# Kernel tuning notes

Measured on AMD Instinct MI355X. Metric: run time of the kernel, lower is better.

The kernel has to match this reference:

```python
import jax, jax.numpy as jnp
import numpy as np

VOCAB, X_SIZE, H_SIZE, N_CLASSES = 50000, 300, 150, 5
DEPTH = 18                      # complete binary tree, N = 2^(DEPTH+1)-1 nodes
N_NODES = 2 ** (DEPTH + 1) - 1  # 524287
SCALE = 0.05                    # param init scale for numerical sanity


def setup_inputs() -> dict:
    key = jax.random.key(0)
    ks = jax.random.split(key, 8)
    return {
        "x_id": jax.random.randint(ks[0], (N_NODES,), 0, VOCAB, dtype=jnp.int32),
        "emb": jax.random.normal(ks[1], (VOCAB, X_SIZE), jnp.float32) * SCALE,
        "W_iou": jax.random.normal(ks[2], (X_SIZE, 3 * H_SIZE), jnp.float32) * SCALE,
        "U_iou": jax.random.normal(ks[3], (H_SIZE, 3 * H_SIZE), jnp.float32) * SCALE,
        "b_iou": jnp.zeros((3 * H_SIZE,), jnp.float32),
        "W_f": jax.random.normal(ks[4], (X_SIZE, H_SIZE), jnp.float32) * SCALE,
        "U_f": jax.random.normal(ks[5], (H_SIZE, H_SIZE), jnp.float32) * SCALE,
        "b_f": jnp.zeros((H_SIZE,), jnp.float32),
        "W_out": jax.random.normal(ks[6], (H_SIZE, N_CLASSES), jnp.float32) * SCALE,
        "b_out": jnp.zeros((N_CLASSES,), jnp.float32),
    }


def reference(x_id, emb, W_iou, U_iou, b_iou, W_f, U_f, b_f, W_out, b_out):
    # Child-Sum TreeLSTM propagated leaves->root over a complete binary tree
    # stored in heap layout: children of node i are 2i+1, 2i+2.
    N = x_id.shape[0]
    H = U_iou.shape[0]
    depth = int(np.log2(N + 1)) - 1

    x = emb[x_id]  # input_module: embedding lookup  [N, X]
    h = jnp.zeros((N, H), x.dtype)
    c = jnp.zeros((N, H), x.dtype)

    # level-batched topological propagation (19 static levels)
    for lvl in range(depth, -1, -1):
        s, e = 2 ** lvl - 1, 2 ** (lvl + 1) - 1  # node range of this level
        xl = x[s:e]                              # [n_l, X]
        if lvl == depth:  # leaves: zero child state
            h_sum = jnp.zeros((e - s, H), x.dtype)
            fc_sum = jnp.zeros((e - s, H), x.dtype)
        else:
            # children of consecutive nodes are contiguous: [2s+1, 2e+1)
            hc = h[2 * s + 1:2 * e + 1].reshape(e - s, 2, H)
            cc = c[2 * s + 1:2 * e + 1].reshape(e - s, 2, H)
            h_sum = hc.sum(axis=1)               # reduce: sum child h
            # per-child forget gate
            f = jax.nn.sigmoid((xl @ W_f)[:, None, :] + hc @ U_f + b_f)
            fc_sum = (f * cc).sum(axis=1)
        iou = xl @ W_iou + h_sum @ U_iou + b_iou  # [n_l, 3H]
        i, o, u = jnp.split(iou, 3, axis=-1)
        c_new = jax.nn.sigmoid(i) * jnp.tanh(u) + fc_sum
        h_new = jax.nn.sigmoid(o) * jnp.tanh(c_new)
        h = h.at[s:e].set(h_new)
        c = c.at[s:e].set(c_new)

    return h @ W_out + b_out  # output_module: Linear(H, C)  [N, C]
```

## Files before the change

### kernel.cpp

```cpp
#include <hip/hip_runtime.h>
#include <cstdint>

typedef _Float16 f16_t;
typedef __attribute__((ext_vector_type(8))) _Float16 f16x8;
typedef __attribute__((ext_vector_type(4))) _Float16 f16x4;
typedef __attribute__((ext_vector_type(4))) float f32x4;

#define HP      160
#define NCOL    640
#define KXP     320
#define NNODES  524287
#define LEAF_S  262143
#define LEAF_M  262144
#define NVOCAB  50000
#define AST     168

__device__ __forceinline__ float frcp(float x) { return __builtin_amdgcn_rcpf(x); }
__device__ __forceinline__ float sigf(float x) { return frcp(1.0f + __expf(-x)); }
__device__ __forceinline__ float tanhf_(float x) {
  return 1.0f - 2.0f * frcp(1.0f + __expf(2.0f * x));
}
__device__ __forceinline__ f16x8 zero8() {
  f16x8 z;
#pragma unroll
  for (int i = 0; i < 8; ++i) z[i] = (_Float16)0.0f;
  return z;
}
__device__ __forceinline__ f32x4 zero4() {
  f32x4 z;
#pragma unroll
  for (int i = 0; i < 4; ++i) z[i] = 0.0f;
  return z;
}

__global__ void prep_params(const float* __restrict__ W_iou, const float* __restrict__ U_iou,
                            const float* __restrict__ b_iou, const float* __restrict__ W_f,
                            const float* __restrict__ U_f, const float* __restrict__ b_f,
                            f16_t* __restrict__ WreT, f16_t* __restrict__ UreT,
                            float* __restrict__ bre) {
  int idx = blockIdx.x * 256 + threadIdx.x;
  if (idx < NCOL * KXP) {
    int col = idx / KXP, k = idx % KXP;
    int j = col >> 2, g = col & 3;
    float v = 0.0f;
    if (k < 300 && j < 150) v = (g < 3) ? W_iou[k * 450 + g * 150 + j] : W_f[k * 150 + j];
    WreT[idx] = (f16_t)v;
  } else if (idx < NCOL * KXP + NCOL * HP) {
    int i2 = idx - NCOL * KXP;
    int col = i2 / HP, k = i2 % HP;
    int g = col / 160, j = col % 160;
    float v = 0.0f;
    if (k < 150 && j < 150) v = (g < 3) ? U_iou[k * 450 + g * 150 + j] : U_f[k * 150 + j];
    UreT[i2] = (f16_t)v;
  } else if (idx < NCOL * KXP + NCOL * HP + NCOL) {
    int col = idx - (NCOL * KXP + NCOL * HP);
    int j = col >> 2, g = col & 3;
    bre[col] = (j < 150) ? ((g < 3) ? b_iou[g * 150 + j] : b_f[j]) : 0.0f;
  }
}

__global__ __launch_bounds__(256) void gemm_p(const float* __restrict__ emb,
                                              const f16_t* __restrict__ WreT,
                                              const float* __restrict__ bre,
                                              f16_t* __restrict__ P) {
  __shared__ __align__(16) f16_t A_sh[64 * 328];
  __shared__ __align__(16) f16_t B_sh[128 * 40];
  const int tid = threadIdx.x;
  const int wid = tid >> 6, lane = tid & 63, l15 = lane & 15, q = lane >> 4;
  const int row0 = blockIdx.x * 64;

#pragma unroll
  for (int i = 0; i < 10; ++i) {
    int ch = tid + 256 * i;
    int r = ch / 40, kc = (ch % 40) * 8;
    int grow = row0 + r;
    f16x8 hv;
    if (grow < NVOCAB && kc + 8 <= 300) {
      float4 a = *(const float4*)&emb[grow * 300 + kc];
      float4 b = *(const float4*)&emb[grow * 300 + kc + 4];
      hv[0] = (_Float16)a.x; hv[1] = (_Float16)a.y; hv[2] = (_Float16)a.z; hv[3] = (_Float16)a.w;
      hv[4] = (_Float16)b.x; hv[5] = (_Float16)b.y; hv[6] = (_Float16)b.z; hv[7] = (_Float16)b.w;
    } else {
#pragma unroll
      for (int e = 0; e < 8; ++e) {
        int k = kc + e;
        float v = (grow < NVOCAB && k < 300) ? emb[grow * 300 + k] : 0.0f;
        hv[e] = (_Float16)v;
      }
    }
    *(f16x8*)&A_sh[r * 328 + kc] = hv;
  }
  __syncthreads();

  for (int bn = 0; bn < 5; ++bn) {
    const int col0 = bn * 128;
    f32x4 acc[8];
#pragma unroll
    for (int t = 0; t < 8; ++t) acc[t] = zero4();
    for (int kk = 0; kk < KXP; kk += 32) {
#pragma unroll
      for (int i = 0; i < 2; ++i) {
        int ch = tid + 256 * i;
        int cidx = ch >> 2, kc = (ch & 3) * 8;
        *(f16x8*)&B_sh[cidx * 40 + kc] =
            *(const f16x8*)&WreT[(col0 + cidx) * KXP + kk + kc];
      }
      __syncthreads();
      f16x8 af = *(const f16x8*)&A_sh[(16 * wid + l15) * 328 + kk + q * 8];
#pragma unroll
      for (int t = 0; t < 8; ++t) {
        f16x8 bfr = *(const f16x8*)&B_sh[(t * 16 + l15) * 40 + q * 8];
        acc[t] = __builtin_amdgcn_mfma_f32_16x16x32_f16(af, bfr, acc[t], 0, 0, 0);
      }
      __syncthreads();
    }
#pragma unroll
    for (int t = 0; t < 8; ++t) {
      int col = col0 + t * 16 + l15;
      float bias = bre[col];
#pragma unroll
      for (int r2 = 0; r2 < 4; ++r2) {
        int row = row0 + 16 * wid + q * 4 + r2;
        if (row < NVOCAB) P[(long)row * NCOL + col] = (f16_t)(acc[t][r2] + bias);
      }
    }
  }
}

__global__ void leafhc_kernel(const f16_t* __restrict__ P, f16_t* __restrict__ Hleaf,
                              f16_t* __restrict__ Cleaf) {
  int idx = blockIdx.x * 256 + threadIdx.x;
  if (idx >= NVOCAB * 80) return;
  int v = idx / 80, t = idx % 80;
  f16x8 pk = *(const f16x8*)&P[(long)v * NCOL + t * 8];
#pragma unroll
  for (int e = 0; e < 2; ++e) {
    float iv = (float)pk[e * 4 + 0], ov = (float)pk[e * 4 + 1], uv = (float)pk[e * 4 + 2];
    float cl = sigf(iv) * tanhf_(uv);
    float hl = sigf(ov) * tanhf_(cl);
    Hleaf[(long)v * HP + t * 2 + e] = (f16_t)hl;
    Cleaf[(long)v * HP + t * 2 + e] = (f16_t)cl;
  }
}

__global__ void oleaf_kernel(const f16_t* __restrict__ Hleaf, const float* __restrict__ W_out,
                             const float* __restrict__ b_out, float* __restrict__ Oleaf) {
  const int tid = threadIdx.x;
  const int row = blockIdx.x * 16 + (tid >> 4), l = tid & 15;
  if (row >= NVOCAB) return;
  float acc[5] = {0, 0, 0, 0, 0};
  for (int j = l; j < 150; j += 16) {
    float hv = (float)Hleaf[(long)row * HP + j];
#pragma unroll
    for (int m = 0; m < 5; ++m) acc[m] += hv * W_out[j * 5 + m];
  }
#pragma unroll
  for (int m = 0; m < 5; ++m) {
    float vv = acc[m];
    vv += __shfl_xor(vv, 1);
    vv += __shfl_xor(vv, 2);
    vv += __shfl_xor(vv, 4);
    vv += __shfl_xor(vv, 8);
    if (l == 0) Oleaf[(long)row * 8 + m] = vv + b_out[m];
  }
}

__global__ void leafout_kernel(const int* __restrict__ x_id, const float* __restrict__ Oleaf,
                               float* __restrict__ out) {
  int leaf = blockIdx.x * 256 + threadIdx.x;
  int xv = x_id[LEAF_S + leaf];
  const float* O = Oleaf + (long)xv * 8;
  float4 o4 = *(const float4*)O;
  float o5 = O[4];
  long base = ((long)LEAF_S + leaf) * 5;
  out[base + 0] = o4.x; out[base + 1] = o4.y; out[base + 2] = o4.z;
  out[base + 3] = o4.w; out[base + 4] = o5;
}

__global__ __launch_bounds__(256, 3) void level17b_kernel(
    const int* __restrict__ x_id, const f16_t* __restrict__ P,
    const f16_t* __restrict__ UreT, const f16_t* __restrict__ Hleaf,
    const f16_t* __restrict__ Cleaf, f16_t* __restrict__ Hout,
    f16_t* __restrict__ Cout, const float* __restrict__ W_out,
    const float* __restrict__ b_out, float* __restrict__ out) {
  __shared__ __align__(16) f16_t A_sh[128 * AST];
  __shared__ __align__(16) f16_t B_sh[128 * 40];
  const int tid = threadIdx.x;
  const int wid = tid >> 6, lane = tid & 63, l15 = lane & 15, q = lane >> 4;
  const int p0 = blockIdx.x * 64;
  const int s1 = (1 << 17) - 1;
  const long childbase = 2L * s1 + 1 + 2 * p0;

#pragma unroll
  for (int i = 0; i < 10; ++i) {
    int ch = tid + 256 * i;
    int r = ch / 20, kc = (ch % 20) * 8;
    int xv = x_id[childbase + r];
    *(f16x8*)&A_sh[r * AST + kc] = *(const f16x8*)&Hleaf[(long)xv * HP + kc];
  }
  __syncthreads();

  int xvp[2][2], xvl[2][2], xvr[2][2];
#pragma unroll
  for (int mt = 0; mt < 2; ++mt)
#pragma unroll
    for (int rr = 0; rr < 2; ++rr) {
      int pl = 16 * wid + 8 * mt + 2 * q + rr;
      xvp[mt][rr] = x_id[(long)s1 + p0 + pl];
      xvl[mt][rr] = x_id[childbase + 2 * pl];
      xvr[mt][rr] = x_id[childbase + 2 * pl + 1];
    }
  float oacc[2][2][5] = {};

  for (int jt = 0; jt < 5; ++jt) {
    const int j0 = jt * 32;
    f32x4 acc[2][4][2];
#pragma unroll
    for (int mt = 0; mt < 2; ++mt)
#pragma unroll
      for (int g = 0; g < 4; ++g)
#pragma unroll
        for (int jh = 0; jh < 2; ++jh) acc[mt][g][jh] = zero4();

    for (int kk = 0; kk < HP; kk += 32) {
#pragma unroll
      for (int i = 0; i < 2; ++i) {
        int ch = tid + 256 * i;
        int cidx = ch >> 2, kc = (ch & 3) * 8;
        int g = cidx >> 5, jj = cidx & 31;
        int col = g * HP + j0 + jj;
        *(f16x8*)&B_sh[cidx * 40 + kc] = *(const f16x8*)&UreT[col * HP + kk + kc];
      }
      __syncthreads();
      f16x8 af0 = *(const f16x8*)&A_sh[(32 * wid + l15) * AST + kk + q * 8];
      f16x8 af1 = *(const f16x8*)&A_sh[(32 * wid + 16 + l15) * AST + kk + q * 8];
#pragma unroll
      for (int g = 0; g < 4; ++g)
#pragma unroll
        for (int jh = 0; jh < 2; ++jh) {
          f16x8 bfr = *(const f16x8*)&B_sh[(g * 32 + jh * 16 + l15) * 40 + q * 8];
          acc[0][g][jh] = __builtin_amdgcn_mfma_f32_16x16x32_f16(af0, bfr, acc[0][g][jh], 0, 0, 0);
          acc[1][g][jh] = __builtin_amdgcn_mfma_f32_16x16x32_f16(af1, bfr, acc[1][g][jh], 0, 0, 0);
        }
      __syncthreads();
    }

#pragma unroll
    for (int mt = 0; mt < 2; ++mt)
#pragma unroll
      for (int rr = 0; rr < 2; ++rr) {
        const int r = rr * 2;
        const int pl = 16 * wid + 8 * mt + 2 * q + rr;
        const f16_t* Prp = P + (long)xvp[mt][rr] * NCOL;
#pragma unroll
        for (int jh = 0; jh < 2; ++jh) {
          const int j = j0 + jh * 16 + l15;
          f16x4 pp = *(const f16x4*)&Prp[j * 4];
          float ipre = (float)pp[0] + acc[mt][0][jh][r] + acc[mt][0][jh][r + 1];
          float opre = (float)pp[1] + acc[mt][1][jh][r] + acc[mt][1][jh][r + 1];
          float upre = (float)pp[2] + acc[mt][2][jh][r] + acc[mt][2][jh][r + 1];
          float pf   = (float)pp[3];
          float fl = sigf(pf + acc[mt][3][jh][r]);
          float fr = sigf(pf + acc[mt][3][jh][r + 1]);
          float clv = (float)Cleaf[(long)xvl[mt][rr] * HP + j];
          float crv = (float)Cleaf[(long)xvr[mt][rr] * HP + j];
          float cn = sigf(ipre) * tanhf_(upre) + fl * clv + fr * crv;
          float hn = sigf(opre) * tanhf_(cn);
          Hout[(long)(p0 + pl) * HP + j] = (f16_t)hn;
          Cout[(long)(p0 + pl) * HP + j] = (f16_t)cn;
          int wbase = (j < 150) ? j * 5 : 0;
#pragma unroll
          for (int m = 0; m < 5; ++m) oacc[mt][rr][m] += hn * W_out[wbase + m];
        }
      }
  }

#pragma unroll
  for (int mt = 0; mt < 2; ++mt)
#pragma unroll
    for (int rr = 0; rr < 2; ++rr) {
      int pl = 16 * wid + 8 * mt + 2 * q + rr;
#pragma unroll
      for (int m = 0; m < 5; ++m) {
        float v = oacc[mt][rr][m];
        v += __shfl_xor(v, 1);
        v += __shfl_xor(v, 2);
        v += __shfl_xor(v, 4);
        v += __shfl_xor(v, 8);
        if (l15 == 0) out[((long)s1 + p0 + pl) * 5 + m] = v + b_out[m];
      }
    }
}

template <bool LEAF>
__global__ __launch_bounds__(256, 3) void fused_kernel(
    const int* __restrict__ x_id, const f16_t* __restrict__ P,
    const f16_t* __restrict__ UreT, const f16_t* __restrict__ Hc,
    const f16_t* __restrict__ Cc, f16_t* __restrict__ Hout,
    f16_t* __restrict__ Cout, const float* __restrict__ W_out,
    const float* __restrict__ b_out, float* __restrict__ out, int s1, int M1) {
  __shared__ __align__(16) f16_t A_sh[64 * AST];
  __shared__ __align__(16) f16_t A2_sh[32 * AST];
  __shared__ __align__(16) f16_t B_sh[128 * 40];
  __shared__ f16_t C_sh[32 * 160];
  const int tid = threadIdx.x;
  const int wid = tid >> 6, lane = tid & 63, l15 = lane & 15, q = lane >> 4;
  const int p0 = blockIdx.x * 32;
  const long childbase = 2L * s1 + 1 + 2 * p0;

#pragma unroll
  for (int i = 0; i < 5; ++i) {
    int ch = tid + 256 * i;
    int r = ch / 20, kc = (ch % 20) * 8;
    f16x8 v;
    if (LEAF) {
      int xv = x_id[childbase + r];
      v = *(const f16x8*)&Hc[(long)xv * HP + kc];
    } else {
      v = *(const f16x8*)&Hc[(long)(2 * p0 + r) * HP + kc];
    }
    *(f16x8*)&A_sh[r * AST + kc] = v;
  }
  __syncthreads();

  int xvp[2], xvl[2], xvr[2];
#pragma unroll
  for (int rr = 0; rr < 2; ++rr) {
    int pl = 8 * wid + 2 * q + rr;
    long pn = (long)s1 + p0 + pl;
    xvp[rr] = x_id[pn];
    if (LEAF) {
      xvl[rr] = x_id[childbase + 2 * pl];
      xvr[rr] = x_id[childbase + 2 * pl + 1];
    }
  }
  float oacc1[2][5] = {};

  for (int jt = 0; jt < 5; ++jt) {
    const int j0 = jt * 32;
    f32x4 acc[4][2];
#pragma unroll
    for (int g = 0; g < 4; ++g)
#pragma unroll
      for (int jh = 0; jh < 2; ++jh) acc[g][jh] = zero4();

    for (int kk = 0; kk < HP; kk += 32) {
#pragma unroll
      for (int i = 0; i < 2; ++i) {
        int ch = tid + 256 * i;
        int cidx = ch >> 2, kc = (ch & 3) * 8;
        int g = cidx >> 5, jj = cidx & 31;
        int col = g * HP + j0 + jj;
        *(f16x8*)&B_sh[cidx * 40 + kc] = *(const f16x8*)&UreT[col * HP + kk + kc];
      }
      __syncthreads();
      f16x8 af = *(const f16x8*)&A_sh[(16 * wid + l15) * AST + kk + q * 8];
#pragma unroll
      for (int g = 0; g < 4; ++g)
#pragma unroll
        for (int jh = 0; jh < 2; ++jh) {
          f16x8 bfr = *(const f16x8*)&B_sh[(g * 32 + jh * 16 + l15) * 40 + q * 8];
          acc[g][jh] = __builtin_amdgcn_mfma_f32_16x16x32_f16(af, bfr, acc[g][jh], 0, 0, 0);
        }
      __syncthreads();
    }

#pragma unroll
    for (int rr = 0; rr < 2; ++rr) {
      const int r = rr * 2;
      const int lr0 = 16 * wid + q * 4 + r;
      const int pl = lr0 >> 1;
      const f16_t* Prp = P + (long)xvp[rr] * NCOL;
#pragma unroll
      for (int jh = 0; jh < 2; ++jh) {
        const int j = j0 + jh * 16 + l15;
        f16x4 pp = *(const f16x4*)&Prp[j * 4];
        float ipre = (float)pp[0] + acc[0][jh][r] + acc[0][jh][r + 1];
        float opre = (float)pp[1] + acc[1][jh][r] + acc[1][jh][r + 1];
        float upre = (float)pp[2] + acc[2][jh][r] + acc[2][jh][r + 1];
        float pf   = (float)pp[3];
        float fl = sigf(pf + acc[3][jh][r]);
        float fr = sigf(pf + acc[3][jh][r + 1]);
        float clv, crv;
        if (LEAF) {
          clv = (float)Cc[(long)xvl[rr] * HP + j];
          crv = (float)Cc[(long)xvr[rr] * HP + j];
        } else {
          clv = (float)Cc[(long)(2 * p0 + lr0) * HP + j];
          crv = (float)Cc[(long)(2 * p0 + lr0 + 1) * HP + j];
        }
        float cn = sigf(ipre) * tanhf_(upre) + fl * clv + fr * crv;
        float hn = sigf(opre) * tanhf_(cn);
        A2_sh[pl * AST + j] = (f16_t)hn;
        C_sh[pl * 160 + j] = (f16_t)cn;
        int wbase = (j < 150) ? j * 5 : 0;
#pragma unroll
        for (int m = 0; m < 5; ++m) oacc1[rr][m] += hn * W_out[wbase + m];
      }
    }
  }

#pragma unroll
  for (int rr = 0; rr < 2; ++rr) {
    int pl = 8 * wid + 2 * q + rr;
#pragma unroll
    for (int m = 0; m < 5; ++m) {
      float v = oacc1[rr][m];
      v += __shfl_xor(v, 1);
      v += __shfl_xor(v, 2);
      v += __shfl_xor(v, 4);
      v += __shfl_xor(v, 8);
      if (l15 == 0) out[((long)s1 + p0 + pl) * 5 + m] = v + b_out[m];
    }
  }

  const int s2 = (s1 - 1) >> 1;
  const int p02 = p0 >> 1;
  const bool act2 = (wid < 2);
  int xvp2[2];
#pragma unroll
  for (int rr = 0; rr < 2; ++rr) {
    int pl = 8 * wid + 2 * q + rr;
    long pn = (long)s2 + p02 + (act2 ? pl : 0);
    xvp2[rr] = x_id[pn];
  }
  float oacc2[2][5] = {};

  for (int jt = 0; jt < 5; ++jt) {
    const int j0 = jt * 32;
    f32x4 acc[4][2];
#pragma unroll
    for (int g = 0; g < 4; ++g)
#pragma unroll
      for (int jh = 0; jh < 2; ++jh) acc[g][jh] = zero4();

    for (int kk = 0; kk < HP; kk += 32) {
#pragma unroll
      for (int i = 0; i < 2; ++i) {
        int ch = tid + 256 * i;
        int cidx = ch >> 2, kc = (ch & 3) * 8;
        int g = cidx >> 5, jj = cidx & 31;
        int col = g * HP + j0 + jj;
        *(f16x8*)&B_sh[cidx * 40 + kc] = *(const f16x8*)&UreT[col * HP + kk + kc];
      }
      __syncthreads();
      if (act2) {
        f16x8 af = *(const f16x8*)&A2_sh[(16 * wid + l15) * AST + kk + q * 8];
#pragma unroll
        for (int g = 0; g < 4; ++g)
#pragma unroll
          for (int jh = 0; jh < 2; ++jh) {
            f16x8 bfr = *(const f16x8*)&B_sh[(g * 32 + jh * 16 + l15) * 40 + q * 8];
            acc[g][jh] = __builtin_amdgcn_mfma_f32_16x16x32_f16(af, bfr, acc[g][jh], 0, 0, 0);
          }
      }
      __syncthreads();
    }

    if (act2) {
#pragma unroll
      for (int rr = 0; rr < 2; ++rr) {
        const int r = rr * 2;
        const int lr0 = 16 * wid + q * 4 + r;
        const int pl = lr0 >> 1;
        const f16_t* Prp = P + (long)xvp2[rr] * NCOL;
#pragma unroll
        for (int jh = 0; jh < 2; ++jh) {
          const int j = j0 + jh * 16 + l15;
          f16x4 pp = *(const f16x4*)&Prp[j * 4];
          float ipre = (float)pp[0] + acc[0][jh][r] + acc[0][jh][r + 1];
          float opre = (float)pp[1] + acc[1][jh][r] + acc[1][jh][r + 1];
          float upre = (float)pp[2] + acc[2][jh][r] + acc[2][jh][r + 1];
          float pf   = (float)pp[3];
          float fl = sigf(pf + acc[3][jh][r]);
          float fr = sigf(pf + acc[3][jh][r + 1]);
          float clv = (float)C_sh[lr0 * 160 + j];
          float crv = (float)C_sh[(lr0 + 1) * 160 + j];
          float cn = sigf(ipre) * tanhf_(upre) + fl * clv + fr * crv;
          float hn = sigf(opre) * tanhf_(cn);
          Hout[(long)(p02 + pl) * HP + j] = (f16_t)hn;
          Cout[(long)(p02 + pl) * HP + j] = (f16_t)cn;
          int wbase = (j < 150) ? j * 5 : 0;
#pragma unroll
          for (int m = 0; m < 5; ++m) oacc2[rr][m] += hn * W_out[wbase + m];
        }
      }
    }
  }

  if (act2) {
#pragma unroll
    for (int rr = 0; rr < 2; ++rr) {
      int pl = 8 * wid + 2 * q + rr;
#pragma unroll
      for (int m = 0; m < 5; ++m) {
        float v = oacc2[rr][m];
        v += __shfl_xor(v, 1);
        v += __shfl_xor(v, 2);
        v += __shfl_xor(v, 4);
        v += __shfl_xor(v, 8);
        if (l15 == 0) out[((long)s2 + p02 + pl) * 5 + m] = v + b_out[m];
      }
    }
  }
}

__device__ __forceinline__ void level_tile(
    const int* __restrict__ x_id, const f16_t* __restrict__ P,
    const f16_t* __restrict__ UreT, const f16_t* __restrict__ h_child,
    const f16_t* __restrict__ c_child, f16_t* __restrict__ h_par,
    f16_t* __restrict__ c_par, const float* Wo, const float* __restrict__ b_out,
    float* __restrict__ out, int s, int M, int p0, f16_t* A_sh, f16_t* B_sh) {
  const int tid = threadIdx.x;
  const int wid = tid >> 6, lane = tid & 63, l15 = lane & 15, q = lane >> 4;
  int rowsValid = 2 * M - 2 * p0;
  if (rowsValid > 64) rowsValid = 64;

#pragma unroll
  for (int i = 0; i < 5; ++i) {
    int ch = tid + 256 * i;
    int r = ch / 20, kc = (ch % 20) * 8;
    f16x8 v;
    if (r < rowsValid) v = *(const f16x8*)&h_child[(long)(2 * p0 + r) * HP + kc];
    else v = zero8();
    *(f16x8*)&A_sh[r * 184 + kc] = v;
  }
  __syncthreads();

  int xvp[2]; long pnode[2]; int plg[2]; bool valid[2]; int lr0v[2];
#pragma unroll
  for (int rr = 0; rr < 2; ++rr) {
    int lr0 = 16 * wid + q * 4 + rr * 2;
    int pl = lr0 >> 1;
    valid[rr] = (p0 + pl) < M;
    long pn = (long)s + p0 + (valid[rr] ? pl : 0);
    pnode[rr] = pn; plg[rr] = p0 + pl; lr0v[rr] = lr0;
    xvp[rr] = x_id[pn];
  }

  float oacc[2][5];
#pragma unroll
  for (int rr = 0; rr < 2; ++rr)
#pragma unroll
    for (int m = 0; m < 5; ++m) oacc[rr][m] = 0.0f;

  for (int jt = 0; jt < 5; ++jt) {
    const int j0 = jt * 32;
    f32x4 acc[4][2];
#pragma unroll
    for (int g = 0; g < 4; ++g)
#pragma unroll
      for (int jh = 0; jh < 2; ++jh) acc[g][jh] = zero4();

    for (int kk = 0; kk < HP; kk += 32) {
#pragma unroll
      for (int i = 0; i < 2; ++i) {
        int ch = tid + 256 * i;
        int cidx = ch >> 2, kc = (ch & 3) * 8;
        int g = cidx >> 5, jj = cidx & 31;
        int col = g * HP + j0 + jj;
        *(f16x8*)&B_sh[cidx * 40 + kc] = *(const f16x8*)&UreT[col * HP + kk + kc];
      }
      __syncthreads();
      f16x8 af = *(const f16x8*)&A_sh[(16 * wid + l15) * 184 + kk + q * 8];
#pragma unroll
      for (int g = 0; g < 4; ++g)
#pragma unroll
        for (int jh = 0; jh < 2; ++jh) {
          f16x8 bfr = *(const f16x8*)&B_sh[(g * 32 + jh * 16 + l15) * 40 + q * 8];
          acc[g][jh] = __builtin_amdgcn_mfma_f32_16x16x32_f16(af, bfr, acc[g][jh], 0, 0, 0);
        }
      __syncthreads();
    }

#pragma unroll
    for (int rr = 0; rr < 2; ++rr) {
      const int r = rr * 2;
      const f16_t* Prp = P + (long)xvp[rr] * NCOL;
#pragma unroll
      for (int jh = 0; jh < 2; ++jh) {
        const int j = j0 + jh * 16 + l15;
        f16x4 pp = *(const f16x4*)&Prp[j * 4];
        float ipre = (float)pp[0] + acc[0][jh][r] + acc[0][jh][r + 1];
        float opre = (float)pp[1] + acc[1][jh][r] + acc[1][jh][r + 1];
        float upre = (float)pp[2] + acc[2][jh][r] + acc[2][jh][r + 1];
        float pf   = (float)pp[3];
        float fl = sigf(pf + acc[3][jh][r]);
        float fr = sigf(pf + acc[3][jh][r + 1]);
        float clv = valid[rr] ? (float)c_child[(long)(2 * p0 + lr0v[rr]) * HP + j] : 0.0f;
        float crv = valid[rr] ? (float)c_child[(long)(2 * p0 + lr0v[rr] + 1) * HP + j] : 0.0f;
        float cn = sigf(ipre) * tanhf_(upre) + fl * clv + fr * crv;
        float hn = sigf(opre) * tanhf_(cn);
        if (valid[rr]) {
          h_par[(long)plg[rr] * HP + j] = (f16_t)hn;
          c_par[(long)plg[rr] * HP + j] = (f16_t)cn;
        }
#pragma unroll
        for (int m = 0; m < 5; ++m) oacc[rr][m] += hn * Wo[j * 5 + m];
      }
    }
  }

#pragma unroll
  for (int rr = 0; rr < 2; ++rr) {
#pragma unroll
    for (int m = 0; m < 5; ++m) {
      float v = oacc[rr][m];
      v += __shfl_xor(v, 1);
      v += __shfl_xor(v, 2);
      v += __shfl_xor(v, 4);
      v += __shfl_xor(v, 8);
      if (l15 == 0 && valid[rr]) out[pnode[rr] * 5 + m] = v + b_out[m];
    }
  }
}

__global__ __launch_bounds__(256, 4) void tail_kernel(
    const int* __restrict__ x_id, const f16_t* __restrict__ P,
    const f16_t* __restrict__ UreT, f16_t* __restrict__ HA, f16_t* __restrict__ HB,
    f16_t* __restrict__ CA, f16_t* __restrict__ CB, const float* __restrict__ W_out,
    const float* __restrict__ b_out, float* __restrict__ out) {
  __shared__ __align__(16) f16_t A_sh[64 * 184];
  __shared__ __align__(16) f16_t B_sh[128 * 40];
  __shared__ float Wo[800];
  for (int i = threadIdx.x; i < 800; i += 256) Wo[i] = (i < 750) ? W_out[i] : 0.0f;
  for (int lvl = 4; lvl >= 0; --lvl) {
    int s = (1 << lvl) - 1, M = 1 << lvl;
    const f16_t* hc = ((lvl + 1) & 1) ? HA : HB;
    const f16_t* cc = ((lvl + 1) & 1) ? CA : CB;
    f16_t* hp = (lvl & 1) ? HA : HB;
    f16_t* cp = (lvl & 1) ? CA : CB;
    level_tile(x_id, P, UreT, hc, cc, hp, cp, Wo, b_out, out, s, M, 0, A_sh, B_sh);
    __syncthreads();
  }
}

extern "C" void kernel_launch(void* const* d_in, const int* in_sizes, int n_in,
                              void* d_out, int out_size, void* d_ws, size_t ws_size,
                              hipStream_t stream) {
  const int* x_id   = (const int*)d_in[0];
  const float* emb  = (const float*)d_in[1];
  const float* W_iou = (const float*)d_in[2];
  const float* U_iou = (const float*)d_in[3];
  const float* b_iou = (const float*)d_in[4];
  const float* W_f   = (const float*)d_in[5];
  const float* U_f   = (const float*)d_in[6];
  const float* b_f   = (const float*)d_in[7];
  const float* W_out = (const float*)d_in[8];
  const float* b_out = (const float*)d_in[9];
  float* out = (float*)d_out;
  char* ws = (char*)d_ws;

  f16_t* WreT  = (f16_t*)(ws + 0);
  f16_t* UreT  = (f16_t*)(ws + 409600);
  float* bre   = (float*)(ws + 614400);
  f16_t* P     = (f16_t*)(ws + 616960);
  f16_t* Hleaf = (f16_t*)(ws + 64616960);
  f16_t* Cleaf = (f16_t*)(ws + 80616960);
  float* Oleaf = (float*)(ws + 96616960);
  f16_t* H17   = (f16_t*)(ws + 96616960);
  f16_t* C17   = (f16_t*)(ws + 138560000);
  f16_t* H15 = (f16_t*)(ws + 64616960);
  f16_t* C15 = (f16_t*)(ws + 75102720);
  f16_t* H13 = (f16_t*)(ws + 96616960);
  f16_t* C13 = (f16_t*)(ws + 99238400);
  f16_t* H11 = (f16_t*)(ws + 64616960);
  f16_t* C11 = (f16_t*)(ws + 65272320);
  f16_t* H9  = (f16_t*)(ws + 96616960);
  f16_t* C9  = (f16_t*)(ws + 96780800);
  f16_t* H7  = (f16_t*)(ws + 64616960);
  f16_t* C7  = (f16_t*)(ws + 64657920);
  f16_t* H5  = (f16_t*)(ws + 96616960);
  f16_t* C5  = (f16_t*)(ws + 96627200);
  f16_t* HSc = (f16_t*)(ws + 64616960);
  f16_t* CSc = (f16_t*)(ws + 64627200);

  prep_params<<<1203, 256, 0, stream>>>(W_iou, U_iou, b_iou, W_f, U_f, b_f, WreT, UreT, bre);
  gemm_p<<<782, 256, 0, stream>>>(emb, WreT, bre, P);
  leafhc_kernel<<<15625, 256, 0, stream>>>(P, Hleaf, Cleaf);
  oleaf_kernel<<<3125, 256, 0, stream>>>(Hleaf, W_out, b_out, Oleaf);
  leafout_kernel<<<1024, 256, 0, stream>>>(x_id, Oleaf, out);

  level17b_kernel<<<2048, 256, 0, stream>>>(x_id, P, UreT, Hleaf, Cleaf, H17, C17,
                                            W_out, b_out, out);
  fused_kernel<false><<<2048, 256, 0, stream>>>(x_id, P, UreT, H17, C17, H15, C15,
                                                W_out, b_out, out, (1 << 16) - 1, 1 << 16);
  fused_kernel<false><<<512, 256, 0, stream>>>(x_id, P, UreT, H15, C15, H13, C13,
                                               W_out, b_out, out, (1 << 14) - 1, 1 << 14);
  fused_kernel<false><<<128, 256, 0, stream>>>(x_id, P, UreT, H13, C13, H11, C11,
                                               W_out, b_out, out, (1 << 12) - 1, 1 << 12);
  fused_kernel<false><<<32, 256, 0, stream>>>(x_id, P, UreT, H11, C11, H9, C9,
                                              W_out, b_out, out, (1 << 10) - 1, 1 << 10);
  fused_kernel<false><<<8, 256, 0, stream>>>(x_id, P, UreT, H9, C9, H7, C7,
                                             W_out, b_out, out, (1 << 8) - 1, 1 << 8);
  fused_kernel<false><<<2, 256, 0, stream>>>(x_id, P, UreT, H7, C7, H5, C5,
                                             W_out, b_out, out, (1 << 6) - 1, 1 << 6);
  tail_kernel<<<1, 256, 0, stream>>>(x_id, P, UreT, H5, HSc, C5, CSc, W_out, b_out, out);

  (void)in_sizes; (void)n_in; (void)out_size; (void)ws_size;
}
```

Before: 814.5 us.

## Fuse leaf h/c/output kernels and widen two-level fused kernel tiles

Merges the leaf h/c kernel and leaf output-projection kernel into one pass over P. The leaf output scatter now runs at the end of the level-17 kernel, and Oleaf moves to its own workspace region. The two-level fused kernel now handles 64 parents per block, so the second level uses all four waves instead of two, with level-one h/c staged in shared memory. This removes two launches and an Hleaf reread and improves wave utilisation, at the cost of more registers (hreg/creg arrays) and half as many blocks per level.

```diff
diff --git a/kernel.cpp b/kernel.cpp
--- a/kernel.cpp
+++ b/kernel.cpp
@@ -4,6 +4,7 @@
 typedef _Float16 f16_t;
 typedef __attribute__((ext_vector_type(8))) _Float16 f16x8;
 typedef __attribute__((ext_vector_type(4))) _Float16 f16x4;
+typedef __attribute__((ext_vector_type(2))) _Float16 f16x2;
 typedef __attribute__((ext_vector_type(4))) float f32x4;
 
 #define HP      160
@@ -127,36 +128,29 @@
   }
 }
 
-__global__ void leafhc_kernel(const f16_t* __restrict__ P, f16_t* __restrict__ Hleaf,
-                              f16_t* __restrict__ Cleaf) {
-  int idx = blockIdx.x * 256 + threadIdx.x;
-  if (idx >= NVOCAB * 80) return;
-  int v = idx / 80, t = idx % 80;
-  f16x8 pk = *(const f16x8*)&P[(long)v * NCOL + t * 8];
-#pragma unroll
-  for (int e = 0; e < 2; ++e) {
-    float iv = (float)pk[e * 4 + 0], ov = (float)pk[e * 4 + 1], uv = (float)pk[e * 4 + 2];
+__global__ void leafhco_kernel(const f16_t* __restrict__ P, const float* __restrict__ W_out,
+                               const float* __restrict__ b_out, f16_t* __restrict__ Hleaf,
+                               f16_t* __restrict__ Cleaf, float* __restrict__ Oleaf) {
+  const int tid = threadIdx.x;
+  const int row = blockIdx.x * 16 + (tid >> 4), l = tid & 15;
+  const f16_t* Pr = P + (long)row * NCOL;
+  float oacc[5] = {0, 0, 0, 0, 0};
+#pragma unroll
+  for (int jj = 0; jj < 10; ++jj) {
+    int j = jj * 16 + l;
+    f16x4 pp = *(const f16x4*)&Pr[j * 4];
+    float iv = (float)pp[0], ov = (float)pp[1], uv = (float)pp[2];
     float cl = sigf(iv) * tanhf_(uv);
     float hl = sigf(ov) * tanhf_(cl);
-    Hleaf[(long)v * HP + t * 2 + e] = (f16_t)hl;
-    Cleaf[(long)v * HP + t * 2 + e] = (f16_t)cl;
-  }
-}
-
-__global__ void oleaf_kernel(const f16_t* __restrict__ Hleaf, const float* __restrict__ W_out,
-                             const float* __restrict__ b_out, float* __restrict__ Oleaf) {
-  const int tid = threadIdx.x;
-  const int row = blockIdx.x * 16 + (tid >> 4), l = tid & 15;
-  if (row >= NVOCAB) return;
-  float acc[5] = {0, 0, 0, 0, 0};
-  for (int j = l; j < 150; j += 16) {
-    float hv = (float)Hleaf[(long)row * HP + j];
-#pragma unroll
-    for (int m = 0; m < 5; ++m) acc[m] += hv * W_out[j * 5 + m];
+    Hleaf[(long)row * HP + j] = (f16_t)hl;
+    Cleaf[(long)row * HP + j] = (f16_t)cl;
+    int wbase = (j < 150) ? j * 5 : 0;
+#pragma unroll
+    for (int m = 0; m < 5; ++m) oacc[m] += hl * W_out[wbase + m];
   }
 #pragma unroll
   for (int m = 0; m < 5; ++m) {
-    float vv = acc[m];
+    float vv = oacc[m];
     vv += __shfl_xor(vv, 1);
     vv += __shfl_xor(vv, 2);
     vv += __shfl_xor(vv, 4);
@@ -165,24 +159,13 @@
   }
 }
 
-__global__ void leafout_kernel(const int* __restrict__ x_id, const float* __restrict__ Oleaf,
-                               float* __restrict__ out) {
-  int leaf = blockIdx.x * 256 + threadIdx.x;
-  int xv = x_id[LEAF_S + leaf];
-  const float* O = Oleaf + (long)xv * 8;
-  float4 o4 = *(const float4*)O;
-  float o5 = O[4];
-  long base = ((long)LEAF_S + leaf) * 5;
-  out[base + 0] = o4.x; out[base + 1] = o4.y; out[base + 2] = o4.z;
-  out[base + 3] = o4.w; out[base + 4] = o5;
-}
-
 __global__ __launch_bounds__(256, 3) void level17b_kernel(
     const int* __restrict__ x_id, const f16_t* __restrict__ P,
     const f16_t* __restrict__ UreT, const f16_t* __restrict__ Hleaf,
-    const f16_t* __restrict__ Cleaf, f16_t* __restrict__ Hout,
-    f16_t* __restrict__ Cout, const float* __restrict__ W_out,
-    const float* __restrict__ b_out, float* __restrict__ out) {
+    const f16_t* __restrict__ Cleaf, const float* __restrict__ Oleaf,
+    f16_t* __restrict__ Hout, f16_t* __restrict__ Cout,
+    const float* __restrict__ W_out, const float* __restrict__ b_out,
+    float* __restrict__ out) {
   __shared__ __align__(16) f16_t A_sh[128 * AST];
   __shared__ __align__(16) f16_t B_sh[128 * 40];
   const int tid = threadIdx.x;
@@ -290,59 +273,60 @@
         if (l15 == 0) out[((long)s1 + p0 + pl) * 5 + m] = v + b_out[m];
       }
     }
-}
-
-template <bool LEAF>
-__global__ __launch_bounds__(256, 3) void fused_kernel(
+
+  if (tid < 128) {
+    long leaf = childbase + tid;
+    int xv = x_id[leaf];
+    const float* O = Oleaf + (long)xv * 8;
+    float4 o4 = *(const float4*)O;
+    float o5 = O[4];
+    long base = leaf * 5;
+    out[base + 0] = o4.x; out[base + 1] = o4.y; out[base + 2] = o4.z;
+    out[base + 3] = o4.w; out[base + 4] = o5;
+  }
+}
+
+__global__ __launch_bounds__(256, 3) void fusedb_kernel(
     const int* __restrict__ x_id, const f16_t* __restrict__ P,
     const f16_t* __restrict__ UreT, const f16_t* __restrict__ Hc,
     const f16_t* __restrict__ Cc, f16_t* __restrict__ Hout,
     f16_t* __restrict__ Cout, const float* __restrict__ W_out,
-    const float* __restrict__ b_out, float* __restrict__ out, int s1, int M1) {
-  __shared__ __align__(16) f16_t A_sh[64 * AST];
-  __shared__ __align__(16) f16_t A2_sh[32 * AST];
+    const float* __restrict__ b_out, float* __restrict__ out, int s1) {
+  __shared__ __align__(16) f16_t A_sh[128 * AST];
   __shared__ __align__(16) f16_t B_sh[128 * 40];
-  __shared__ f16_t C_sh[32 * 160];
   const int tid = threadIdx.x;
   const int wid = tid >> 6, lane = tid & 63, l15 = lane & 15, q = lane >> 4;
-  const int p0 = blockIdx.x * 32;
-  const long childbase = 2L * s1 + 1 + 2 * p0;
-
-#pragma unroll
-  for (int i = 0; i < 5; ++i) {
+  const int p0 = blockIdx.x * 64;
+
+#pragma unroll
+  for (int i = 0; i < 10; ++i) {
     int ch = tid + 256 * i;
     int r = ch / 20, kc = (ch % 20) * 8;
-    f16x8 v;
-    if (LEAF) {
-      int xv = x_id[childbase + r];
-      v = *(const f16x8*)&Hc[(long)xv * HP + kc];
-    } else {
-      v = *(const f16x8*)&Hc[(long)(2 * p0 + r) * HP + kc];
-    }
-    *(f16x8*)&A_sh[r * AST + kc] = v;
+    *(f16x8*)&A_sh[r * AST + kc] = *(const f16x8*)&Hc[(long)(2 * p0 + r) * HP + kc];
   }
   __syncthreads();
 
-  int xvp[2], xvl[2], xvr[2];
-#pragma unroll
-  for (int rr = 0; rr < 2; ++rr) {
-    int pl = 8 * wid + 2 * q + rr;
-    long pn = (long)s1 + p0 + pl;
-    xvp[rr] = x_id[pn];
-    if (LEAF) {
-      xvl[rr] = x_id[childbase + 2 * pl];
-      xvr[rr] = x_id[childbase + 2 * pl + 1];
-    }
-  }
-  float oacc1[2][5] = {};
-
+  int xvp[2][2];
+#pragma unroll
+  for (int mt = 0; mt < 2; ++mt)
+#pragma unroll
+    for (int rr = 0; rr < 2; ++rr) {
+      int pl = 16 * wid + 8 * mt + 2 * q + rr;
+      xvp[mt][rr] = x_id[(long)s1 + p0 + pl];
+    }
+  f16x2 hreg[5][2][2];
+  f16x2 creg[5][2][2];
+
+#pragma unroll
   for (int jt = 0; jt < 5; ++jt) {
     const int j0 = jt * 32;
-    f32x4 acc[4][2];
-#pragma unroll
-    for (int g = 0; g < 4; ++g)
-#pragma unroll
-      for (int jh = 0; jh < 2; ++jh) acc[g][jh] = zero4();
+    f32x4 acc[2][4][2];
+#pragma unroll
+    for (int mt = 0; mt < 2; ++mt)
+#pragma unroll
+      for (int g = 0; g < 4; ++g)
+#pragma unroll
+        for (int jh = 0; jh < 2; ++jh) acc[mt][g][jh] = zero4();
 
     for (int kk = 0; kk < HP; kk += 32) {
 #pragma unroll
@@ -354,6 +338,122 @@
         *(f16x8*)&B_sh[cidx * 40 + kc] = *(const f16x8*)&UreT[col * HP + kk + kc];
       }
       __syncthreads();
+      f16x8 af0 = *(const f16x8*)&A_sh[(32 * wid + l15) * AST + kk + q * 8];
+      f16x8 af1 = *(const f16x8*)&A_sh[(32 * wid + 16 + l15) * AST + kk + q * 8];
+#pragma unroll
+      for (int g = 0; g < 4; ++g)
+#pragma unroll
+        for (int jh = 0; jh < 2; ++jh) {
+          f16x8 bfr = *(const f16x8*)&B_sh[(g * 32 + jh * 16 + l15) * 40 + q * 8];
+          acc[0][g][jh] = __builtin_amdgcn_mfma_f32_16x16x32_f16(af0, bfr, acc[0][g][jh], 0, 0, 0);
+          acc[1][g][jh] = __builtin_amdgcn_mfma_f32_16x16x32_f16(af1, bfr, acc[1][g][jh], 0, 0, 0);
+        }
+      __syncthreads();
+    }
+
+#pragma unroll
+    for (int mt = 0; mt < 2; ++mt)
+#pragma unroll
+      for (int rr = 0; rr < 2; ++rr) {
+        const int r = rr * 2;
+        const int lr0 = 32 * wid + 16 * mt + 4 * q + r;
+        const f16_t* Prp = P + (long)xvp[mt][rr] * NCOL;
+#pragma unroll
+        for (int jh = 0; jh < 2; ++jh) {
+          const int j = j0 + jh * 16 + l15;
+          f16x4 pp = *(const f16x4*)&Prp[j * 4];
+          float ipre = (float)pp[0] + acc[mt][0][jh][r] + acc[mt][0][jh][r + 1];
+          float opre = (float)pp[1] + acc[mt][1][jh][r] + acc[mt][1][jh][r + 1];
+          float upre = (float)pp[2] + acc[mt][2][jh][r] + acc[mt][2][jh][r + 1];
+          float pf   = (float)pp[3];
+          float fl = sigf(pf + acc[mt][3][jh][r]);
+          float fr = sigf(pf + acc[mt][3][jh][r + 1]);
+          float clv = (float)Cc[(long)(2 * p0 + lr0) * HP + j];
+          float crv = (float)Cc[(long)(2 * p0 + lr0 + 1) * HP + j];
+          float cn = sigf(ipre) * tanhf_(upre) + fl * clv + fr * crv;
+          float hn = sigf(opre) * tanhf_(cn);
+          hreg[jt][mt][rr][jh] = (_Float16)hn;
+          creg[jt][mt][rr][jh] = (_Float16)cn;
+        }
+      }
+  }
+
+#pragma unroll
+  for (int jt = 0; jt < 5; ++jt)
+#pragma unroll
+    for (int mt = 0; mt < 2; ++mt)
+#pragma unroll
+      for (int rr = 0; rr < 2; ++rr) {
+        const int pl = 16 * wid + 8 * mt + 2 * q + rr;
+#pragma unroll
+        for (int jh = 0; jh < 2; ++jh) {
+          const int j = jt * 32 + jh * 16 + l15;
+          A_sh[pl * AST + j] = hreg[jt][mt][rr][jh];
+          A_sh[(64 + pl) * AST + j] = creg[jt][mt][rr][jh];
+        }
+      }
+
+  {
+    float oacc1[2][2][5] = {};
+#pragma unroll
+    for (int jt = 0; jt < 5; ++jt)
+#pragma unroll
+      for (int mt = 0; mt < 2; ++mt)
+#pragma unroll
+        for (int rr = 0; rr < 2; ++rr)
+#pragma unroll
+          for (int jh = 0; jh < 2; ++jh) {
+            const int j = jt * 32 + jh * 16 + l15;
+            float hn = (float)hreg[jt][mt][rr][jh];
+            int wbase = (j < 150) ? j * 5 : 0;
+#pragma unroll
+            for (int m = 0; m < 5; ++m) oacc1[mt][rr][m] += hn * W_out[wbase + m];
+          }
+#pragma unroll
+    for (int mt = 0; mt < 2; ++mt)
+#pragma unroll
+      for (int rr = 0; rr < 2; ++rr) {
+        int pl = 16 * wid + 8 * mt + 2 * q + rr;
+#pragma unroll
+        for (int m = 0; m < 5; ++m) {
+          float v = oacc1[mt][rr][m];
+          v += __shfl_xor(v, 1);
+          v += __shfl_xor(v, 2);
+          v += __shfl_xor(v, 4);
+          v += __shfl_xor(v, 8);
+          if (l15 == 0) out[((long)s1 + p0 + pl) * 5 + m] = v + b_out[m];
+        }
+      }
+  }
+
+  const int s2 = (s1 - 1) >> 1;
+  const int p02 = p0 >> 1;
+  int xvp2[2];
+#pragma unroll
+  for (int rr = 0; rr < 2; ++rr) {
+    int pl2 = 8 * wid + 2 * q + rr;
+    xvp2[rr] = x_id[(long)s2 + p02 + pl2];
+  }
+  float oacc2[2][5] = {};
+
+  for (int jt = 0; jt < 5; ++jt) {
+    const int j0 = jt * 32;
+    f32x4 acc[4][2];
+#pragma unroll
+    for (int g = 0; g < 4; ++g)
+#pragma unroll
+      for (int jh = 0; jh < 2; ++jh) acc[g][jh] = zero4();
+
+    for (int kk = 0; kk < HP; kk += 32) {
+#pragma unroll
+      for (int i = 0; i < 2; ++i) {
+        int ch = tid + 256 * i;
+        int cidx = ch >> 2, kc = (ch & 3) * 8;
+        int g = cidx >> 5, jj = cidx & 31;
+        int col = g * HP + j0 + jj;
+        *(f16x8*)&B_sh[cidx * 40 + kc] = *(const f16x8*)&UreT[col * HP + kk + kc];
+      }
+      __syncthreads();
       f16x8 af = *(const f16x8*)&A_sh[(16 * wid + l15) * AST + kk + q * 8];
 #pragma unroll
       for (int g = 0; g < 4; ++g)
@@ -368,9 +468,9 @@
 #pragma unroll
     for (int rr = 0; rr < 2; ++rr) {
       const int r = rr * 2;
-      const int lr0 = 16 * wid + q * 4 + r;
-      const int pl = lr0 >> 1;
-      const f16_t* Prp = P + (long)xvp[rr] * NCOL;
+      const int lr0 = 16 * wid + 4 * q + r;
+      const int pl2 = lr0 >> 1;
+      const f16_t* Prp = P + (long)xvp2[rr] * NCOL;
 #pragma unroll
       for (int jh = 0; jh < 2; ++jh) {
         const int j = j0 + jh * 16 + l15;
@@ -381,126 +481,30 @@
         float pf   = (float)pp[3];
         float fl = sigf(pf + acc[3][jh][r]);
         float fr = sigf(pf + acc[3][jh][r + 1]);
-        float clv, crv;
-        if (LEAF) {
-          clv = (float)Cc[(long)xvl[rr] * HP + j];
-          crv = (float)Cc[(long)xvr[rr] * HP + j];
-        } else {
-          clv = (float)Cc[(long)(2 * p0 + lr0) * HP + j];
-          crv = (float)Cc[(long)(2 * p0 + lr0 + 1) * HP + j];
-        }
+        float clv = (float)A_sh[(64 + lr0) * AST + j];
+        float crv = (float)A_sh[(64 + lr0 + 1) * AST + j];
         float cn = sigf(ipre) * tanhf_(upre) + fl * clv + fr * crv;
         float hn = sigf(opre) * tanhf_(cn);
-        A2_sh[pl * AST + j] = (f16_t)hn;
-        C_sh[pl * 160 + j] = (f16_t)cn;
+        Hout[(long)(p02 + pl2) * HP + j] = (f16_t)hn;
+        Cout[(long)(p02 + pl2) * HP + j] = (f16_t)cn;
         int wbase = (j < 150) ? j * 5 : 0;
 #pragma unroll
-        for (int m = 0; m < 5; ++m) oacc1[rr][m] += hn * W_out[wbase + m];
+        for (int m = 0; m < 5; ++m) oacc2[rr][m] += hn * W_out[wbase + m];
       }
     }
   }
 
 #pragma unroll
   for (int rr = 0; rr < 2; ++rr) {
-    int pl = 8 * wid + 2 * q + rr;
+    int pl2 = 8 * wid + 2 * q + rr;
 #pragma unroll
     for (int m = 0; m < 5; ++m) {
-      float v = oacc1[rr][m];
+      float v = oacc2[rr][m];
       v += __shfl_xor(v, 1);
       v += __shfl_xor(v, 2);
       v += __shfl_xor(v, 4);
       v += __shfl_xor(v, 8);
-      if (l15 == 0) out[((long)s1 + p0 + pl) * 5 + m] = v + b_out[m];
-    }
-  }
-
-  const int s2 = (s1 - 1) >> 1;
-  const int p02 = p0 >> 1;
-  const bool act2 = (wid < 2);
-  int xvp2[2];
-#pragma unroll
-  for (int rr = 0; rr < 2; ++rr) {
-    int pl = 8 * wid + 2 * q + rr;
-    long pn = (long)s2 + p02 + (act2 ? pl : 0);
-    xvp2[rr] = x_id[pn];
-  }
-  float oacc2[2][5] = {};
-
-  for (int jt = 0; jt < 5; ++jt) {
-    const int j0 = jt * 32;
-    f32x4 acc[4][2];
-#pragma unroll
-    for (int g = 0; g < 4; ++g)
-#pragma unroll
-      for (int jh = 0; jh < 2; ++jh) acc[g][jh] = zero4();
-
-    for (int kk = 0; kk < HP; kk += 32) {
-#pragma unroll
-      for (int i = 0; i < 2; ++i) {
-        int ch = tid + 256 * i;
-        int cidx = ch >> 2, kc = (ch & 3) * 8;
-        int g = cidx >> 5, jj = cidx & 31;
-        int col = g * HP + j0 + jj;
-        *(f16x8*)&B_sh[cidx * 40 + kc] = *(const f16x8*)&UreT[col * HP + kk + kc];
-      }
-      __syncthreads();
-      if (act2) {
-        f16x8 af = *(const f16x8*)&A2_sh[(16 * wid + l15) * AST + kk + q * 8];
-#pragma unroll
-        for (int g = 0; g < 4; ++g)
-#pragma unroll
-          for (int jh = 0; jh < 2; ++jh) {
-            f16x8 bfr = *(const f16x8*)&B_sh[(g * 32 + jh * 16 + l15) * 40 + q * 8];
-            acc[g][jh] = __builtin_amdgcn_mfma_f32_16x16x32_f16(af, bfr, acc[g][jh], 0, 0, 0);
-          }
-      }
-      __syncthreads();
-    }
-
-    if (act2) {
-#pragma unroll
-      for (int rr = 0; rr < 2; ++rr) {
-        const int r = rr * 2;
-        const int lr0 = 16 * wid + q * 4 + r;
-        const int pl = lr0 >> 1;
-        const f16_t* Prp = P + (long)xvp2[rr] * NCOL;
-#pragma unroll
-        for (int jh = 0; jh < 2; ++jh) {
-          const int j = j0 + jh * 16 + l15;
-          f16x4 pp = *(const f16x4*)&Prp[j * 4];
-          float ipre = (float)pp[0] + acc[0][jh][r] + acc[0][jh][r + 1];
-          float opre = (float)pp[1] + acc[1][jh][r] + acc[1][jh][r + 1];
-          float upre = (float)pp[2] + acc[2][jh][r] + acc[2][jh][r + 1];
-          float pf   = (float)pp[3];
-          float fl = sigf(pf + acc[3][jh][r]);
-          float fr = sigf(pf + acc[3][jh][r + 1]);
-          float clv = (float)C_sh[lr0 * 160 + j];
-          float crv = (float)C_sh[(lr0 + 1) * 160 + j];
-          float cn = sigf(ipre) * tanhf_(upre) + fl * clv + fr * crv;
-          float hn = sigf(opre) * tanhf_(cn);
-          Hout[(long)(p02 + pl) * HP + j] = (f16_t)hn;
-          Cout[(long)(p02 + pl) * HP + j] = (f16_t)cn;
-          int wbase = (j < 150) ? j * 5 : 0;
-#pragma unroll
-          for (int m = 0; m < 5; ++m) oacc2[rr][m] += hn * W_out[wbase + m];
-        }
-      }
-    }
-  }
-
-  if (act2) {
-#pragma unroll
-    for (int rr = 0; rr < 2; ++rr) {
-      int pl = 8 * wid + 2 * q + rr;
-#pragma unroll
-      for (int m = 0; m < 5; ++m) {
-        float v = oacc2[rr][m];
-        v += __shfl_xor(v, 1);
-        v += __shfl_xor(v, 2);
-        v += __shfl_xor(v, 4);
-        v += __shfl_xor(v, 8);
-        if (l15 == 0) out[((long)s2 + p02 + pl) * 5 + m] = v + b_out[m];
-      }
+      if (l15 == 0) out[((long)s2 + p02 + pl2) * 5 + m] = v + b_out[m];
     }
   }
 }
@@ -657,9 +661,9 @@
   f16_t* P     = (f16_t*)(ws + 616960);
   f16_t* Hleaf = (f16_t*)(ws + 64616960);
   f16_t* Cleaf = (f16_t*)(ws + 80616960);
-  float* Oleaf = (float*)(ws + 96616960);
   f16_t* H17   = (f16_t*)(ws + 96616960);
   f16_t* C17   = (f16_t*)(ws + 138560000);
+  float* Oleaf = (float*)(ws + 180503040);
   f16_t* H15 = (f16_t*)(ws + 64616960);
   f16_t* C15 = (f16_t*)(ws + 75102720);
   f16_t* H13 = (f16_t*)(ws + 96616960);
@@ -677,24 +681,22 @@
 
   prep_params<<<1203, 256, 0, stream>>>(W_iou, U_iou, b_iou, W_f, U_f, b_f, WreT, UreT, bre);
   gemm_p<<<782, 256, 0, stream>>>(emb, WreT, bre, P);
-  leafhc_kernel<<<15625, 256, 0, stream>>>(P, Hleaf, Cleaf);
-  oleaf_kernel<<<3125, 256, 0, stream>>>(Hleaf, W_out, b_out, Oleaf);
-  leafout_kernel<<<1024, 256, 0, stream>>>(x_id, Oleaf, out);
-
-  level17b_kernel<<<2048, 256, 0, stream>>>(x_id, P, UreT, Hleaf, Cleaf, H17, C17,
-                                            W_out, b_out, out);
-  fused_kernel<false><<<2048, 256, 0, stream>>>(x_id, P, UreT, H17, C17, H15, C15,
-                                                W_out, b_out, out, (1 << 16) - 1, 1 << 16);
-  fused_kernel<false><<<512, 256, 0, stream>>>(x_id, P, UreT, H15, C15, H13, C13,
-                                               W_out, b_out, out, (1 << 14) - 1, 1 << 14);
-  fused_kernel<false><<<128, 256, 0, stream>>>(x_id, P, UreT, H13, C13, H11, C11,
-                                               W_out, b_out, out, (1 << 12) - 1, 1 << 12);
-  fused_kernel<false><<<32, 256, 0, stream>>>(x_id, P, UreT, H11, C11, H9, C9,
-                                              W_out, b_out, out, (1 << 10) - 1, 1 << 10);
-  fused_kernel<false><<<8, 256, 0, stream>>>(x_id, P, UreT, H9, C9, H7, C7,
-                                             W_out, b_out, out, (1 << 8) - 1, 1 << 8);
-  fused_kernel<false><<<2, 256, 0, stream>>>(x_id, P, UreT, H7, C7, H5, C5,
-                                             W_out, b_out, out, (1 << 6) - 1, 1 << 6);
+  leafhco_kernel<<<3125, 256, 0, stream>>>(P, W_out, b_out, Hleaf, Cleaf, Oleaf);
+
+  level17b_kernel<<<2048, 256, 0, stream>>>(x_id, P, UreT, Hleaf, Cleaf, Oleaf,
+                                            H17, C17, W_out, b_out, out);
+  fusedb_kernel<<<1024, 256, 0, stream>>>(x_id, P, UreT, H17, C17, H15, C15,
+                                          W_out, b_out, out, (1 << 16) - 1);
+  fusedb_kernel<<<256, 256, 0, stream>>>(x_id, P, UreT, H15, C15, H13, C13,
+                                         W_out, b_out, out, (1 << 14) - 1);
+  fusedb_kernel<<<64, 256, 0, stream>>>(x_id, P, UreT, H13, C13, H11, C11,
+                                        W_out, b_out, out, (1 << 12) - 1);
+  fusedb_kernel<<<16, 256, 0, stream>>>(x_id, P, UreT, H11, C11, H9, C9,
+                                        W_out, b_out, out, (1 << 10) - 1);
+  fusedb_kernel<<<4, 256, 0, stream>>>(x_id, P, UreT, H9, C9, H7, C7,
+                                       W_out, b_out, out, (1 << 8) - 1);
+  fusedb_kernel<<<1, 256, 0, stream>>>(x_id, P, UreT, H7, C7, H5, C5,
+                                       W_out, b_out, out, (1 << 6) - 1);
   tail_kernel<<<1, 256, 0, stream>>>(x_id, P, UreT, H5, HSc, C5, CSc, W_out, b_out, out);
 
   (void)in_sizes; (void)n_in; (void)out_size; (void)ws_size;
```

Result: slower. 987.6 us (+21.2%).
